# Kernel tuning notes

Hardware: AMD Instinct MI355X
Metric: run time of the kernel (lower is better)

## Reference

```python
import jax, jax.numpy as jnp
import numpy as np

E, N, D, H, F, M, L = 4, 2048, 256, 8, 2048, 4096, 3
GAMMA = 0.1
EPS = 1e-5  # torch LayerNorm default


def setup_inputs() -> dict:
    key = jax.random.key(0)
    ks = jax.random.split(key, 8)
    s = 0.02  # keep randn-initialized weights in a sane range
    return {
        "tokens": jax.random.normal(ks[0], (E, N, D), jnp.float32),
        "memories": jax.random.normal(ks[1], (L, M, D), jnp.float32),
        "in_proj_w": jax.random.normal(ks[2], (E, 3 * D, D), jnp.float32) * s,
        "in_proj_b": jnp.zeros((E, 3 * D), jnp.float32),
        "out_w": jax.random.normal(ks[3], (E, D, D), jnp.float32) * s,
        "out_b": jnp.zeros((E, D), jnp.float32),
        "lin1_w": jax.random.normal(ks[4], (E, F, D), jnp.float32) * s,
        "lin1_b": jnp.zeros((E, F), jnp.float32),
        "lin2_w": jax.random.normal(ks[5], (E, D, F), jnp.float32) * s,
        "lin2_b": jnp.zeros((E, D), jnp.float32),
        "ln1_w": jnp.ones((E, D), jnp.float32),
        "ln1_b": jnp.zeros((E, D), jnp.float32),
        "ln2_w": jnp.ones((E, D), jnp.float32),
        "ln2_b": jnp.zeros((E, D), jnp.float32),
        "agg_w": jax.random.normal(ks[6], (D, L * D), jnp.float32) * s,
        "agg_b": jnp.zeros((D,), jnp.float32),
        "global_gate": jax.random.normal(ks[7], (D, 1), jnp.float32),
    }


def _ln(x, g, b):
    mu = x.mean(-1, keepdims=True)
    var = ((x - mu) ** 2).mean(-1, keepdims=True)
    return (x - mu) * jax.lax.rsqrt(var + EPS) * g + b


def _mha(x, wqkv, bqkv, wo, bo):
    # unbatched nn.MultiheadAttention, self-attention, eval mode (no dropout)
    qkv = x @ wqkv.T + bqkv                          # [N, 3D]
    q, k, v = jnp.split(qkv, 3, axis=-1)
    hd = D // H
    q = q.reshape(-1, H, hd)
    k = k.reshape(-1, H, hd)
    v = v.reshape(-1, H, hd)
    att = jax.nn.softmax(jnp.einsum('nhd,mhd->hnm', q, k) / jnp.sqrt(jnp.float32(hd)), axis=-1)
    o = jnp.einsum('hnm,mhd->nhd', att, v).reshape(-1, D)
    return o @ wo.T + bo


def _forward(tokens, memories, in_proj_w, in_proj_b, out_w, out_b,
             lin1_w, lin1_b, lin2_w, lin2_b, ln1_w, ln1_b, ln2_w, ln2_b,
             agg_w, agg_b, global_gate):
    scale = 1.0 / jnp.sqrt(jnp.float32(D))
    # context for expert i = concat of all other experts' tokens  [E, (E-1)*N, D]
    contexts = jnp.stack([
        jnp.concatenate([tokens[j] for j in range(E) if j != i], axis=0)
        for i in range(E)
    ])

    def per_expert(tok, ctx, wqkv, bqkv, wo, bo, w1, b1, w2, b2, g1, be1, g2, be2):
        # cross-expert attention
        ca = jax.nn.softmax(tok @ ctx.T * scale, axis=-1) @ ctx
        x = tok + ca
        # one post-norm TransformerEncoderLayer (relu FFN, eval mode)
        x = _ln(x + _mha(x, wqkv, bqkv, wo, bo), g1, be1)
        x = _ln(x + (jax.nn.relu(x @ w1.T + b1) @ w2.T + b2), g2, be2)
        # multi-layer memory read + write accumulation
        scores = jax.nn.softmax(jnp.einsum('nd,lmd->lnm', x, memories) * scale, axis=-1)
        ret = jnp.einsum('lnm,lmd->lnd', scores, memories)        # [L, N, D]
        upd = jnp.einsum('lnm,nd->lmd', scores, x)                # [L, M, D]
        multi = ret.transpose(1, 0, 2).reshape(N, L * D) @ agg_w.T + agg_b
        return x + multi, upd

    expert_out, upds = jax.vmap(per_expert)(
        tokens, contexts, in_proj_w, in_proj_b, out_w, out_b,
        lin1_w, lin1_b, lin2_w, lin2_b, ln1_w, ln1_b, ln2_w, ln2_b)
    # EMA memory update (torch.no_grad -> stop_gradient)
    new_memories = jax.lax.stop_gradient((1.0 - GAMMA) * memories + GAMMA * upds.sum(0))
    # gated fusion
    pooled = expert_out.mean(axis=1)                              # [E, D]
    gate_weights = jax.nn.softmax((pooled @ global_gate).squeeze(-1), axis=0)
    fused = jnp.einsum('e,end->nd', gate_weights, expert_out)     # [N, D]
    return fused, gate_weights, new_memories


def reference(tokens, memories, in_proj_w, in_proj_b, out_w, out_b,
              lin1_w, lin1_b, lin2_w, lin2_b, ln1_w, ln1_b, ln2_w, ln2_b,
              agg_w, agg_b, global_gate):
    return _forward(tokens, memories, in_proj_w, in_proj_b, out_w, out_b,
                    lin1_w, lin1_b, lin2_w, lin2_b, ln1_w, ln1_b, ln2_w, ln2_b,
                    agg_w, agg_b, global_gate)
```

## Files before the change

kernel.cpp:

```cpp
#include <hip/hip_runtime.h>
#include <hip/hip_bf16.h>
#include <math.h>

#define E_ 4
#define N_ 2048
#define D_ 256
#define H_ 8
#define F_ 2048
#define M_ 4096
#define L_ 3
#define GAMMA_ 0.1f
#define EPS_ 1e-5f
#define CCH 8

#define GF_ATOMIC 1
#define GF_RELU   2

typedef __attribute__((ext_vector_type(8))) short  sh8;
typedef __attribute__((ext_vector_type(4))) float  fx4;
typedef __hip_bfloat16 bf16;

#define MFMA16 __builtin_amdgcn_mfma_f32_16x16x32_bf16

__device__ inline void gload_lds16(const void* g, void* l) {
    __builtin_amdgcn_global_load_lds((const __attribute__((address_space(1))) void*)g,
                                     (__attribute__((address_space(3))) void*)l, 16, 0, 0);
}

__device__ inline void stage_k64(const bf16* __restrict__ gbase, bf16* lds, int tid) {
    #pragma unroll
    for (int i = 0; i < 8; ++i) {
        int q = i * 256 + tid;
        int row = q >> 5, cst = q & 31;
        int cl = cst ^ (row & 7);
        gload_lds16((const char*)gbase + row * 512 + cl * 16, (char*)lds + q * 16);
    }
}
__device__ inline sh8 ldsK(const bf16* lds, int row, int ks, int hi) {
    return *(const sh8*)((const char*)lds + row * 512 + (((ks * 4 + hi) ^ (row & 7)) << 4));
}

__device__ inline void stage_v64(const bf16* __restrict__ gbase, long rstride, bf16* lds, int tid) {
    #pragma unroll
    for (int i = 0; i < 8; ++i) {
        int q = i * 256 + tid;
        int row = q >> 3, cst = q & 7;
        int cl = cst ^ (row & 7);
        gload_lds16((const char*)(gbase + (long)row * rstride + cl * 8), (char*)lds + q * 16);
    }
}
__device__ inline sh8 ldsV(const bf16* lds, int row, int ks, int hi) {
    return *(const sh8*)((const char*)lds + row * 128 + (((ks * 4 + hi) ^ (row & 7)) << 4));
}

template<int BN>
__global__ __launch_bounds__(256, 4)
void gemm_bf16(const bf16* __restrict__ A, int lda,
               const bf16* __restrict__ Bt, int ldb, long wstride,
               float* C, int ldc, bf16* Cbf,
               int M, int N, int K, int Kc,
               float alpha, const float* __restrict__ bias, long bstride,
               const float* res, int ldres, int flags,
               const bf16* __restrict__ zerobuf)
{
    constexpr int MI  = (BN == 128) ? 4 : 2;
    constexpr int BCH = BN * 8 / 256;
    __shared__ char smem[16384 + BN * 128];
    char* sA = smem;
    char* sB = smem + 16384;
    const int tid  = threadIdx.x;
    const int lane = tid & 63;
    const int lo   = lane & 15, hi = lane >> 4;
    const int wid  = tid >> 6;
    const int rowbase = (BN == 128) ? (wid >> 1) * 64 : wid * 32;
    const int colbase = (BN == 128) ? (wid & 1) * 64 : 0;
    const int bm = blockIdx.y * 128, bn = blockIdx.x * BN;

    const int eid = (blockIdx.y * 128) >> 11;
    const bf16* Bte = Bt + (long)eid * wstride;
    const float* biase = bias ? (bias + (long)eid * bstride) : nullptr;

    const int kbeg = blockIdx.z * Kc;
    const int kend = min(K, kbeg + Kc);

    fx4 acc[MI][4] = {};

    for (int k0 = kbeg; k0 < kend; k0 += 64) {
        #pragma unroll
        for (int i = 0; i < 4; ++i) {
            int id  = i * 256 + tid;
            int row = id >> 3;
            int c   = (id & 7) ^ (row & 7);
            int gk  = k0 + c * 8;
            const bf16* gp = (gk < kend) ? (A + (long)(bm + row) * lda + gk) : zerobuf;
            gload_lds16(gp, sA + id * 16);
        }
        #pragma unroll
        for (int i = 0; i < BCH; ++i) {
            int id  = i * 256 + tid;
            int row = id >> 3;
            int c   = (id & 7) ^ (row & 7);
            int gk  = k0 + c * 8;
            const bf16* gp = (gk < kend && bn + row < N) ? (Bte + (long)(bn + row) * ldb + gk)
                                                         : zerobuf;
            gload_lds16(gp, sB + id * 16);
        }
        asm volatile("s_waitcnt vmcnt(0)" ::: "memory");
        __syncthreads();

        #pragma unroll
        for (int kk = 0; kk < 2; ++kk) {
            const int ko = kk * 32 + hi * 8;
            sh8 af[MI], bfr[4];
            #pragma unroll
            for (int i = 0; i < MI; ++i) {
                int row = rowbase + i * 16 + lo;
                int off = (row * 128 + ko * 2) ^ ((row & 7) << 4);
                af[i] = *(const sh8*)(sA + off);
            }
            #pragma unroll
            for (int j = 0; j < 4; ++j) {
                int row = colbase + j * 16 + lo;
                int off = (row * 128 + ko * 2) ^ ((row & 7) << 4);
                bfr[j] = *(const sh8*)(sB + off);
            }
            #pragma unroll
            for (int i = 0; i < MI; ++i)
                #pragma unroll
                for (int j = 0; j < 4; ++j)
                    acc[i][j] = MFMA16(af[i], bfr[j], acc[i][j], 0, 0, 0);
        }
        __syncthreads();
    }

    const bool z0 = (blockIdx.z == 0);
// ... 32 lines not shown
    const int tid = threadIdx.x, lane = tid & 63, w = tid >> 6;
    const int lo = lane & 15, hi = lane >> 4;
    const float scaleH = 0.17677669529663687f;
    const bf16* qkv_e = qkv + (long)e * N_ * 768;
    const bf16* vT_eh = vT + ((long)e * D_ + h * 32) * N_;
    __shared__ bf16 Plds[4][16][72];

    sh8 qf = *(const sh8*)(qkv_e + (long)(n0 + w * 16 + lo) * 768 + h * 32 + hi * 8);

    float m[4], l[4];
    fx4 acc[2] = {};
    #pragma unroll
    for (int r = 0; r < 4; ++r) { m[r] = -INFINITY; l[r] = 0.f; }

    for (int kc = 0; kc < N_; kc += 64) {
        float sv[4][4], rmax[4], rsum[4];
        #pragma unroll
        for (int j = 0; j < 4; ++j) {
            sh8 kf = *(const sh8*)(qkv_e + (long)(kc + j * 16 + lo) * 768 + 256 + h * 32 + hi * 8);
            fx4 s = {};
            s = MFMA16(qf, kf, s, 0, 0, 0);
            #pragma unroll
            for (int r = 0; r < 4; ++r) sv[j][r] = s[r] * scaleH;
        }
        #pragma unroll
        for (int r = 0; r < 4; ++r)
            rmax[r] = fmaxf(fmaxf(sv[0][r], sv[1][r]), fmaxf(sv[2][r], sv[3][r]));
        #pragma unroll
        for (int d = 1; d < 16; d <<= 1)
            #pragma unroll
            for (int r = 0; r < 4; ++r) rmax[r] = fmaxf(rmax[r], __shfl_xor(rmax[r], d, 64));
        float sc[4];
        #pragma unroll
        for (int r = 0; r < 4; ++r) {
            float mn = fmaxf(m[r], rmax[r]);
            sc[r] = __expf(m[r] - mn);
            m[r] = mn; rsum[r] = 0.f;
        }
        #pragma unroll
        for (int j = 0; j < 4; ++j)
            #pragma unroll
            for (int r = 0; r < 4; ++r) {
                float p = __expf(sv[j][r] - m[r]);
                sv[j][r] = p; rsum[r] += p;
            }
        #pragma unroll
        for (int d = 1; d < 16; d <<= 1)
            #pragma unroll
            for (int r = 0; r < 4; ++r) rsum[r] += __shfl_xor(rsum[r], d, 64);
        #pragma unroll
        for (int r = 0; r < 4; ++r) l[r] = l[r] * sc[r] + rsum[r];
        #pragma unroll
        for (int j2 = 0; j2 < 2; ++j2)
            #pragma unroll
            for (int r = 0; r < 4; ++r) acc[j2][r] *= sc[r];
        #pragma unroll
        for (int j = 0; j < 4; ++j)
            #pragma unroll
            for (int r = 0; r < 4; ++r)
                Plds[w][hi * 4 + r][j * 16 + lo] = __float2bfloat16(sv[j][r]);
        asm volatile("s_waitcnt lgkmcnt(0)" ::: "memory");
        __builtin_amdgcn_sched_barrier(0);
        __builtin_amdgcn_s_setprio(1);
        #pragma unroll
        for (int ks = 0; ks < 2; ++ks) {
            sh8 pa = *(const sh8*)(&Plds[w][lo][ks * 32 + hi * 8]);
            #pragma unroll
            for (int j2 = 0; j2 < 2; ++j2) {
                sh8 vb = *(const sh8*)(vT_eh + (long)(j2 * 16 + lo) * N_ + kc + ks * 32 + hi * 8);
                acc[j2] = MFMA16(pa, vb, acc[j2], 0, 0, 0);
            }
        }
        __builtin_amdgcn_s_setprio(0);
    }
    #pragma unroll
    for (int j2 = 0; j2 < 2; ++j2)
        #pragma unroll
        for (int r = 0; r < 4; ++r) {
            long row = (long)e * N_ + n0 + w * 16 + hi * 4 + r;
            obuf[row * D_ + h * 32 + j2 * 16 + lo] = __float2bfloat16(acc[j2][r] / l[r]);
        }
}

__global__ __launch_bounds__(256, 2)
void flash_cross(const bf16* __restrict__ tok, const bf16* __restrict__ tokT,
                 bf16* __restrict__ Opart, float2* __restrict__ ml)
{
    const int e = blockIdx.z, ch = blockIdx.y;
    const int n0 = blockIdx.x * 64;
    const int tid = threadIdx.x, lane = tid & 63, w = tid >> 6;
    const int lo = lane & 15, hi = lane >> 4;
    const float scaleD = 1.0f / 16.0f;
    __shared__ bf16 Kt[64 * 256];
    __shared__ bf16 Vt[256 * 64];
    __shared__ bf16 Plds[4][16][72];

    sh8 qf[8];
    {
        const bf16* qr = tok + ((long)e * N_ + n0 + w * 16 + lo) * D_;
        #pragma unroll
        for (int ks = 0; ks < 8; ++ks) qf[ks] = *(const sh8*)(qr + ks * 32 + hi * 8);
    }
    float m[4], l[4];
    fx4 acc[16] = {};
    #pragma unroll
    for (int r = 0; r < 4; ++r) { m[r] = -INFINITY; l[r] = 0.f; }

    for (int kc = ch * 768; kc < ch * 768 + 768; kc += 64) {
        const int seg = kc >> 11;
        const int src = (seg < e) ? seg : seg + 1;
        const int rowb = kc & 2047;
        stage_k64(tok + ((long)src * N_ + rowb) * D_, Kt, tid);
        stage_v64(tokT + (long)src * D_ * N_ + rowb, N_, Vt, tid);
        asm volatile("s_waitcnt vmcnt(0)" ::: "memory");
        __syncthreads();

        float sv[4][4], rmax[4], rsum[4];
        __builtin_amdgcn_s_setprio(1);
        #pragma unroll
        for (int j = 0; j < 4; ++j) {
            int krow = j * 16 + lo;
            fx4 s = {};
            #pragma unroll
            for (int ks = 0; ks < 8; ++ks) {
                sh8 kf = ldsK(Kt, krow, ks, hi);
                s = MFMA16(qf[ks], kf, s, 0, 0, 0);
            }
            #pragma unroll
            for (int r = 0; r < 4; ++r) sv[j][r] = s[r] * scaleD;
        }
        __builtin_amdgcn_s_setprio(0);
        #pragma unroll
        for (int r = 0; r < 4; ++r)
            rmax[r] = fmaxf(fmaxf(sv[0][r], sv[1][r]), fmaxf(sv[2][r], sv[3][r]));
        #pragma unroll
        for (int d = 1; d < 16; d <<= 1)
            #pragma unroll
            for (int r = 0; r < 4; ++r) rmax[r] = fmaxf(rmax[r], __shfl_xor(rmax[r], d, 64));
        float sc[4];
        #pragma unroll
        for (int r = 0; r < 4; ++r) {
            float mn = fmaxf(m[r], rmax[r]);
            sc[r] = __expf(m[r] - mn);
            m[r] = mn; rsum[r] = 0.f;
        }
        #pragma unroll
        for (int j = 0; j < 4; ++j)
            #pragma unroll
            for (int r = 0; r < 4; ++r) {
                float p = __expf(sv[j][r] - m[r]);
                sv[j][r] = p; rsum[r] += p;
            }
        #pragma unroll
        for (int d = 1; d < 16; d <<= 1)
            #pragma unroll
            for (int r = 0; r < 4; ++r) rsum[r] += __shfl_xor(rsum[r], d, 64);
        #pragma unroll
        for (int r = 0; r < 4; ++r) l[r] = l[r] * sc[r] + rsum[r];
        #pragma unroll
        for (int j2 = 0; j2 < 16; ++j2)
            #pragma unroll
            for (int r = 0; r < 4; ++r) acc[j2][r] *= sc[r];
        #pragma unroll
        for (int j = 0; j < 4; ++j)
            #pragma unroll
            for (int r = 0; r < 4; ++r)
                Plds[w][hi * 4 + r][j * 16 + lo] = __float2bfloat16(sv[j][r]);
        asm volatile("s_waitcnt lgkmcnt(0)" ::: "memory");
        __builtin_amdgcn_sched_barrier(0);
        __builtin_amdgcn_s_setprio(1);
        #pragma unroll
        for (int ks = 0; ks < 2; ++ks) {
            sh8 pa = *(const sh8*)(&Plds[w][lo][ks * 32 + hi * 8]);
            #pragma unroll
            for (int j2 = 0; j2 < 16; ++j2) {
                sh8 vb = ldsV(Vt, j2 * 16 + lo, ks, hi);
                acc[j2] = MFMA16(pa, vb, acc[j2], 0, 0, 0);
            }
        }
        __builtin_amdgcn_s_setprio(0);
        __syncthreads();
    }
    const long base = (long)ch * E_ * N_ + (long)e * N_ + n0 + w * 16;
    #pragma unroll
    for (int j2 = 0; j2 < 16; ++j2)
        #pragma unroll
        for (int r = 0; r < 4; ++r)
            Opart[(base + hi * 4 + r) * D_ + j2 * 16 + lo] = __float2bfloat16(acc[j2][r] / l[r]);
    if (lo == 0) {
        #pragma unroll
        for (int r = 0; r < 4; ++r) {
            float2 t; t.x = m[r]; t.y = l[r];
            ml[base + hi * 4 + r] = t;
        }
    }
}

__global__ void cross_merge(const bf16* __restrict__ Opart, const float2* __restrict__ ml,
                            const float* __restrict__ tokens,
                            float* __restrict__ x0f, bf16* __restrict__ x0bf)
{
    long row = blockIdx.x; int d = threadIdx.x;
    float2 v[CCH];
    float mx = -INFINITY;
    #pragma unroll
    for (int i = 0; i < CCH; ++i) { v[i] = ml[(long)i * E_ * N_ + row]; mx = fmaxf(mx, v[i].x); }
    float L = 0.f, o = 0.f;
    #pragma unroll
    for (int i = 0; i < CCH; ++i) {
        float wgt = v[i].y * __expf(v[i].x - mx);
        L += wgt;
        o += wgt * __bfloat162float(Opart[((long)i * E_ * N_ + row) * D_ + d]);
    }
    float val = tokens[row * D_ + d] + o / L;
    x0f[row * D_ + d] = val;
    x0bf[row * D_ + d] = __float2bfloat16(val);
}

__global__ __launch_bounds__(256, 2)
void ret_flash(const bf16* __restrict__ x2b, const bf16* __restrict__ memb,
               const bf16* __restrict__ maggT, bf16* __restrict__ OmemH,
               float* __restrict__ rsH)
{
    const int li = blockIdx.y;
    const int e = blockIdx.z >> 1, mh = blockIdx.z & 1;
    const int n0 = blockIdx.x * 64;
    const int tid = threadIdx.x, lane = tid & 63, w = tid >> 6;
    const int lo = lane & 15, hi = lane >> 4;
    const float scaleD = 1.0f / 16.0f;
    __shared__ bf16 Kt[64 * 256];
    __shared__ bf16 Vt[256 * 64];
    __shared__ bf16 Plds[4][16][72];

    sh8 qf[8];
    {
        const bf16* qr = x2b + ((long)e * N_ + n0 + w * 16 + lo) * D_;
        #pragma unroll
        for (int ks = 0; ks < 8; ++ks) qf[ks] = *(const sh8*)(qr + ks * 32 + hi * 8);
    }
    float l[4] = {0.f, 0.f, 0.f, 0.f};
    fx4 acc[16] = {};
    const bf16* Kl = memb + (long)li * M_ * D_;
    const bf16* Vl = maggT + (long)li * D_ * M_;
    const int mbase = mh * 2048;

    for (int t = 0; t < 32; ++t) {
        const int m0 = mbase + t * 64;
        stage_k64(Kl + (long)m0 * D_, Kt, tid);
        stage_v64(Vl + m0, M_, Vt, tid);
        asm volatile("s_waitcnt vmcnt(0)" ::: "memory");
        __syncthreads();

        float sv[4][4], rsum[4] = {0.f, 0.f, 0.f, 0.f};
        __builtin_amdgcn_s_setprio(1);
        #pragma unroll
        for (int j = 0; j < 4; ++j) {
            int krow = j * 16 + lo;
            fx4 s = {};
            #pragma unroll
            for (int ks = 0; ks < 8; ++ks) {
                sh8 kf = ldsK(Kt, krow, ks, hi);
                s = MFMA16(qf[ks], kf, s, 0, 0, 0);
            }
            #pragma unroll
            for (int r = 0; r < 4; ++r) {
                float p = __expf(s[r] * scaleD);
                sv[j][r] = p; rsum[r] += p;
            }
        }
        __builtin_amdgcn_s_setprio(0);
        #pragma unroll
        for (int d = 1; d < 16; d <<= 1)
            #pragma unroll
            for (int r = 0; r < 4; ++r) rsum[r] += __shfl_xor(rsum[r], d, 64);
        #pragma unroll
        for (int r = 0; r < 4; ++r) l[r] += rsum[r];
        #pragma unroll
        for (int j = 0; j < 4; ++j)
            #pragma unroll
            for (int r = 0; r < 4; ++r)
                Plds[w][hi * 4 + r][j * 16 + lo] = __float2bfloat16(sv[j][r]);
        asm volatile("s_waitcnt lgkmcnt(0)" ::: "memory");
        __builtin_amdgcn_sched_barrier(0);
        __builtin_amdgcn_s_setprio(1);
        #pragma unroll
        for (int ks = 0; ks < 2; ++ks) {
            sh8 pa = *(const sh8*)(&Plds[w][lo][ks * 32 + hi * 8]);
            #pragma unroll
            for (int j2 = 0; j2 < 16; ++j2) {
                sh8 vb = ldsV(Vt, j2 * 16 + lo, ks, hi);
                acc[j2] = MFMA16(pa, vb, acc[j2], 0, 0, 0);
            }
        }
        __builtin_amdgcn_s_setprio(0);
        __syncthreads();
    }
    const long rowb = ((long)(mh * 12 + e * L_ + li)) * N_ + n0 + w * 16;
    #pragma unroll
    for (int j2 = 0; j2 < 16; ++j2)
        #pragma unroll
        for (int r = 0; r < 4; ++r)
            OmemH[(rowb + hi * 4 + r) * D_ + j2 * 16 + lo] = __float2bfloat16(acc[j2][r]);
    if (lo == 0) {
        #pragma unroll
        for (int r = 0; r < 4; ++r)
            rsH[rowb + hi * 4 + r] = l[r];
    }
}

__global__ __launch_bounds__(256, 2)
void upd_flash(const bf16* __restrict__ x2b, const bf16* __restrict__ memb,
               const bf16* __restrict__ x2T, const float* __restrict__ rsH,
               bf16* __restrict__ updpart)
{
    const int li = blockIdx.y, e = blockIdx.z;
    const int m0 = blockIdx.x * 64;
    const int tid = threadIdx.x, lane = tid & 63, w = tid >> 6;
    const int lo = lane & 15, hi = lane >> 4;
    const float scaleD = 1.0f / 16.0f;
    __shared__ bf16 Kt[64 * 256];
    __shared__ bf16 Vt[256 * 64];
    __shared__ bf16 Plds[4][16][72];

    sh8 qf[8];
    {
        const bf16* qr = memb + (long)li * M_ * D_ + (long)(m0 + w * 16 + lo) * D_;
        #pragma unroll
        for (int ks = 0; ks < 8; ++ks) qf[ks] = *(const sh8*)(qr + ks * 32 + hi * 8);
    }
    fx4 acc[16] = {};
    const float* rs0 = rsH + (long)(e * L_ + li) * N_;
    const float* rs1 = rsH + (long)(12 + e * L_ + li) * N_;
    const bf16* x2Te = x2T + (long)e * D_ * N_;

    for (int t = 0; t < 32; ++t) {
        const int n0 = t * 64;
        stage_k64(x2b + ((long)e * N_ + n0) * D_, Kt, tid);
        stage_v64(x2Te + n0, N_, Vt, tid);
        float rinv[4];
        #pragma unroll
        for (int j = 0; j < 4; ++j) {
            int n = n0 + j * 16 + lo;
            rinv[j] = 1.0f / (rs0[n] + rs1[n]);
        }
        asm volatile("s_waitcnt vmcnt(0)" ::: "memory");
        __syncthreads();

        __builtin_amdgcn_s_setprio(1);
        #pragma unroll
        for (int j = 0; j < 4; ++j) {
            int krow = j * 16 + lo;
            fx4 s = {};
            #pragma unroll
            for (int ks = 0; ks < 8; ++ks) {
                sh8 kf = ldsK(Kt, krow, ks, hi);
                s = MFMA16(qf[ks], kf, s, 0, 0, 0);
            }
            #pragma unroll
            for (int r = 0; r < 4; ++r) {
                float p = __expf(s[r] * scaleD) * rinv[j];
                Plds[w][hi * 4 + r][j * 16 + lo] = __float2bfloat16(p);
            }
        }
        __builtin_amdgcn_s_setprio(0);
        asm volatile("s_waitcnt lgkmcnt(0)" ::: "memory");
        __builtin_amdgcn_sched_barrier(0);
        __builtin_amdgcn_s_setprio(1);
        #pragma unroll
        for (int ks = 0; ks < 2; ++ks) {
            sh8 pa = *(const sh8*)(&Plds[w][lo][ks * 32 + hi * 8]);
            #pragma unroll
            for (int j2 = 0; j2 < 16; ++j2) {
                sh8 vb = ldsV(Vt, j2 * 16 + lo, ks, hi);
                acc[j2] = MFMA16(pa, vb, acc[j2], 0, 0, 0);
            }
        }
        __builtin_amdgcn_s_setprio(0);
        __syncthreads();
    }
    const long mrow = ((long)(e * L_ + li)) * M_ + m0 + w * 16;
    #pragma unroll
    for (int j2 = 0; j2 < 16; ++j2)
        #pragma unroll
        for (int r = 0; r < 4; ++r)
            updpart[(mrow + hi * 4 + r) * D_ + j2 * 16 + lo] = __float2bfloat16(acc[j2][r]);
}

__global__ void retscale(const bf16* __restrict__ OmemH, const float* __restrict__ rsH,
                         const float* __restrict__ aggb, float* __restrict__ xfinal)
{
    long row = blockIdx.x; int d = threadIdx.x;
    int e = (int)(row >> 11); long n = row & 2047;
    float s = aggb[d];
    #pragma unroll
    for (int li = 0; li < L_; ++li) {
        long r0 = ((long)(e * L_ + li)) * N_ + n;
        long r1 = ((long)(12 + e * L_ + li)) * N_ + n;
        float o = __bfloat162float(OmemH[r0 * D_ + d]) + __bfloat162float(OmemH[r1 * D_ + d]);
        s += o / (rsH[r0] + rsH[r1]);
    }
    xfinal[row * D_ + d] += s;
}

__global__ void layernorm_rows(const float* __restrict__ X, const float* __restrict__ g,
                               const float* __restrict__ b, float* __restrict__ out,
                               bf16* __restrict__ outbf)
{
    __shared__ float red[256];
    int row = blockIdx.x, t = threadIdx.x;
    int e = row >> 11;
    float v = X[(long)row * 256 + t];
    red[t] = v; __syncthreads();
    for (int s = 128; s > 0; s >>= 1) { if (t < s) red[t] += red[t + s]; __syncthreads(); }
    float mu = red[0] * (1.0f / 256.0f); __syncthreads();
    float d = v - mu;
    red[t] = d * d; __syncthreads();
    for (int s = 128; s > 0; s >>= 1) { if (t < s) red[t] += red[t + s]; __syncthreads(); }
    float var = red[0] * (1.0f / 256.0f);
    float o = d * rsqrtf(var + EPS_) * g[e * 256 + t] + b[e * 256 + t];
    out[(long)row * 256 + t] = o;
    outbf[(long)row * 256 + t] = __float2bfloat16(o);
}

__global__ void cvt_bf16(const float* __restrict__ in, bf16* __restrict__ out, long n) {
    long i = ((long)blockIdx.x * 256 + threadIdx.x) * 4;
    if (i < n) {
        float4 v = *(const float4*)(in + i);
        out[i + 0] = __float2bfloat16(v.x);
        out[i + 1] = __float2bfloat16(v.y);
        out[i + 2] = __float2bfloat16(v.z);
        out[i + 3] = __float2bfloat16(v.w);
    }
}

__device__ inline float ldf(const float* p) { return *p; }
__device__ inline float ldf(const bf16* p)  { return __bfloat162float(*p); }

template<typename T>
__global__ void transpose_bf16(const T* __restrict__ in, bf16* __restrict__ out,
                               int R, int C, int ldin, int ldout) {
    __shared__ float t[64][65];
    int tx = threadIdx.x & 63, ty = threadIdx.x >> 6;
    int r0 = blockIdx.y * 64, c0 = blockIdx.x * 64;
    #pragma unroll
    for (int i = 0; i < 16; ++i) {
        int r = ty + i * 4;
        t[r][tx] = ldf(&in[(long)(r0 + r) * ldin + (c0 + tx)]);
    }
    __syncthreads();
    #pragma unroll
    for (int i = 0; i < 16; ++i) {
        int c = ty + i * 4;
        out[(long)(c0 + c) * ldout + (r0 + tx)] = __float2bfloat16(t[tx][c]);
    }
}

__global__ void mem_update(const float4* __restrict__ mem, const bf16* __restrict__ updpart,
                           float4* __restrict__ out) {
    long i = (long)blockIdx.x * 256 + threadIdx.x;
    const long LMD = (long)L_ * M_ * D_;
    if (i < LMD / 4) {
// ... 81 lines not shown
    cvt_bf16<<<dim3((unsigned)((n / 4 + 255) / 256)), dim3(256), 0, s>>>(in, out, n);
}

extern "C" void kernel_launch(void* const* d_in, const int* in_sizes, int n_in,
                              void* d_out, int out_size, void* d_ws, size_t ws_size,
                              hipStream_t stream) {
    const float* tokens    = (const float*)d_in[0];
    const float* memories  = (const float*)d_in[1];
    const float* in_proj_w = (const float*)d_in[2];
    const float* in_proj_b = (const float*)d_in[3];
    const float* out_w     = (const float*)d_in[4];
    const float* out_b     = (const float*)d_in[5];
    const float* lin1_w    = (const float*)d_in[6];
    const float* lin1_b    = (const float*)d_in[7];
    const float* lin2_w    = (const float*)d_in[8];
    const float* lin2_b    = (const float*)d_in[9];
    const float* ln1_w     = (const float*)d_in[10];
    const float* ln1_b     = (const float*)d_in[11];
    const float* ln2_w     = (const float*)d_in[12];
    const float* ln2_b     = (const float*)d_in[13];
    const float* agg_w     = (const float*)d_in[14];
    const float* agg_b     = (const float*)d_in[15];
    const float* gg        = (const float*)d_in[16];

    char* p = (char*)d_ws;
    auto alloc = [&](size_t bytes) { char* r = p; p += (bytes + 255) & ~(size_t)255; return r; };

    char*  regionA = alloc((size_t)32 * 1024 * 1024);
    bf16*  Opart   = (bf16*)regionA;
    bf16*  hid_all = (bf16*)regionA;
    bf16*  OmemH   = (bf16*)regionA;

    char*  regionB = alloc((size_t)32 * 1024 * 1024);
    bf16*  qkv_bf  = (bf16*)regionB;
    bf16*  vT_bf   = (bf16*)(regionB + 12582912);
    bf16*  obuf_bf = (bf16*)(regionB + 12582912 + 4194304);
    bf16*  updpart = (bf16*)regionB;

    float* xfinal  = (float*)alloc((size_t)E_ * N_ * D_ * 4);
    bf16*  x2_bf   = (bf16*)alloc((size_t)E_ * N_ * D_ * 2);
    bf16*  x2T_bf  = (bf16*)alloc((size_t)E_ * D_ * N_ * 2);
    float* x0f     = (float*)alloc((size_t)E_ * N_ * D_ * 4);
    bf16*  x0bf    = (bf16*)alloc((size_t)E_ * N_ * D_ * 2);
    float* ybuf    = (float*)alloc((size_t)E_ * N_ * D_ * 4);
    bf16*  tok_bf  = (bf16*)alloc((size_t)E_ * N_ * D_ * 2);
    bf16*  tokT_bf = (bf16*)alloc((size_t)E_ * D_ * N_ * 2);
    bf16*  mem_bf  = (bf16*)alloc((size_t)L_ * M_ * D_ * 2);
    bf16*  maggT   = (bf16*)alloc((size_t)L_ * D_ * M_ * 2);
    float2* mlbuf  = (float2*)alloc((size_t)CCH * E_ * N_ * sizeof(float2));
    float* rsH     = (float*)alloc((size_t)2 * 12 * N_ * 4);
    bf16*  ipw_bf  = (bf16*)alloc((size_t)E_ * 3 * D_ * D_ * 2);
    bf16*  outw_bf = (bf16*)alloc((size_t)E_ * D_ * D_ * 2);
    bf16*  l1w_bf  = (bf16*)alloc((size_t)E_ * F_ * D_ * 2);
    bf16*  l2w_bf  = (bf16*)alloc((size_t)E_ * D_ * F_ * 2);
    bf16*  aggw_bf = (bf16*)alloc((size_t)D_ * 3 * D_ * 2);
    float* pooled  = (float*)alloc(1024 * 4);
    float* gatebuf = (float*)alloc(64);
    bf16*  zerobuf = (bf16*)alloc(64);

    float* x1f  = x0f;
    bf16*  x1bf = x0bf;

    float* out_fused = (float*)d_out;
    float* out_gate  = out_fused + (long)N_ * D_;
    float* out_mem   = out_gate + E_;

    hipMemsetAsync(zerobuf, 0, 64, stream);
    hipMemsetAsync(pooled, 0, 1024 * 4, stream);

    convert(stream, tokens, tok_bf, (long)E_ * N_ * D_);
    convert(stream, memories, mem_bf, (long)L_ * M_ * D_);
    convert(stream, in_proj_w, ipw_bf, (long)E_ * 3 * D_ * D_);
    convert(stream, out_w, outw_bf, (long)E_ * D_ * D_);
    convert(stream, lin1_w, l1w_bf, (long)E_ * F_ * D_);
    convert(stream, lin2_w, l2w_bf, (long)E_ * D_ * F_);
    convert(stream, agg_w, aggw_bf, (long)D_ * 3 * D_);
    for (int e = 0; e < E_; ++e)
        transposeF(stream, tokens + (long)e * N_ * D_, tokT_bf + (long)e * D_ * N_, N_, D_, D_, N_);
    for (int l = 0; l < L_; ++l)
        gemm(stream, 128, aggw_bf + l * D_, 3 * D_, mem_bf + (long)l * M_ * D_, D_, 0,
             nullptr, M_, maggT + (long)l * D_ * M_, D_, M_, D_, D_,
             1.0f, nullptr, 0, nullptr, 0, 0, zerobuf);

    flash_cross<<<dim3(N_ / 64, CCH, E_), dim3(256), 0, stream>>>(tok_bf, tokT_bf, Opart, mlbuf);
    cross_merge<<<dim3(E_ * N_), dim3(256), 0, stream>>>(Opart, mlbuf, tokens, x0f, x0bf);

    gemm(stream, 128, x0bf, D_, ipw_bf, D_, (long)3 * D_ * D_,
         nullptr, 3 * D_, qkv_bf, E_ * N_, 3 * D_, D_, D_,
         1.0f, in_proj_b, 3 * D_, nullptr, 0, 0, zerobuf);
    for (int e = 0; e < E_; ++e)
        transposeB(stream, qkv_bf + (long)e * N_ * 3 * D_ + 2 * D_, vT_bf + (long)e * D_ * N_,
                   N_, D_, 3 * D_, N_);
    flash_mha<<<dim3(N_ / 64, H_, E_), dim3(256), 0, stream>>>(qkv_bf, vT_bf, obuf_bf);
    gemm(stream, 64, obuf_bf, D_, outw_bf, D_, (long)D_ * D_,
         ybuf, D_, nullptr, E_ * N_, D_, D_, D_,
         1.0f, out_b, D_, x0f, D_, 0, zerobuf);
    layernorm_rows<<<dim3(E_ * N_), dim3(256), 0, stream>>>(ybuf, ln1_w, ln1_b, x1f, x1bf);

    gemm(stream, 128, x1bf, D_, l1w_bf, D_, (long)F_ * D_,
         nullptr, F_, hid_all, E_ * N_, F_, D_, D_,
         1.0f, lin1_b, F_, nullptr, 0, GF_RELU, zerobuf);
    hipMemsetAsync(ybuf, 0, (size_t)E_ * N_ * D_ * 4, stream);
    gemm(stream, 64, hid_all, F_, l2w_bf, F_, (long)D_ * F_,
         ybuf, D_, nullptr, E_ * N_, D_, F_, 512,
         1.0f, lin2_b, D_, x1f, D_, GF_ATOMIC, zerobuf);
    layernorm_rows<<<dim3(E_ * N_), dim3(256), 0, stream>>>(ybuf, ln2_w, ln2_b, xfinal, x2_bf);
    for (int e = 0; e < E_; ++e)
        transposeF(stream, xfinal + (long)e * N_ * D_, x2T_bf + (long)e * D_ * N_, N_, D_, D_, N_);

    ret_flash<<<dim3(N_ / 64, L_, E_ * 2), dim3(256), 0, stream>>>(x2_bf, mem_bf, maggT, OmemH, rsH);
    upd_flash<<<dim3(M_ / 64, L_, E_), dim3(256), 0, stream>>>(x2_bf, mem_bf, x2T_bf, rsH, updpart);
    retscale<<<dim3(E_ * N_), dim3(256), 0, stream>>>(OmemH, rsH, agg_b, xfinal);

    mem_update<<<dim3(L_ * M_ * D_ / 4 / 256), dim3(256), 0, stream>>>(
        (const float4*)memories, updpart, (float4*)out_mem);
    pool_partial<<<dim3(E_, 16), dim3(256), 0, stream>>>(xfinal, pooled);
    gate_kernel<<<dim3(1), dim3(256), 0, stream>>>(pooled, gg, out_gate, gatebuf);
    fuse_kernel<<<dim3((N_ * D_ + 255) / 256), dim3(256), 0, stream>>>(xfinal, gatebuf, out_fused);
}
```

Measured before the change: 876.0 us.

## Double-buffer K/V tiles in flash kernels with 32-row chunks

The three flash-attention style kernels (cross attention, memory retrieval, memory update) now stage K and V in 32-row chunks into two LDS buffers. The next chunk's global-to-LDS loads are issued right after the barrier so they overlap with compute on the current chunk, and the trailing barrier is removed. This targets the load latency that was exposed because each iteration waited on its own loads before computing. The cost is twice as many loop iterations with smaller MFMA batches per iteration and more barrier and softmax bookkeeping overhead. LDS use stays the same size.

```diff
diff --git a/kernel.cpp b/kernel.cpp
--- a/kernel.cpp
+++ b/kernel.cpp
@@ -36,21 +36,30 @@
         gload_lds16((const char*)gbase + row * 512 + cl * 16, (char*)lds + q * 16);
     }
 }
+__device__ inline void stage_k32(const bf16* __restrict__ gbase, bf16* lds, int tid) {
+    #pragma unroll
+    for (int i = 0; i < 4; ++i) {
+        int q = i * 256 + tid;
+        int row = q >> 5, cst = q & 31;
+        int cl = cst ^ (row & 7);
+        gload_lds16((const char*)gbase + row * 512 + cl * 16, (char*)lds + q * 16);
+    }
+}
 __device__ inline sh8 ldsK(const bf16* lds, int row, int ks, int hi) {
     return *(const sh8*)((const char*)lds + row * 512 + (((ks * 4 + hi) ^ (row & 7)) << 4));
 }
 
-__device__ inline void stage_v64(const bf16* __restrict__ gbase, long rstride, bf16* lds, int tid) {
-    #pragma unroll
-    for (int i = 0; i < 8; ++i) {
+__device__ inline void stage_v32(const bf16* __restrict__ gbase, long rstride, bf16* lds, int tid) {
+    #pragma unroll
+    for (int i = 0; i < 4; ++i) {
         int q = i * 256 + tid;
-        int row = q >> 3, cst = q & 7;
-        int cl = cst ^ (row & 7);
+        int row = q >> 2, cst = q & 3;
+        int cl = cst ^ (row & 3);
         gload_lds16((const char*)(gbase + (long)row * rstride + cl * 8), (char*)lds + q * 16);
     }
 }
-__device__ inline sh8 ldsV(const bf16* lds, int row, int ks, int hi) {
-    return *(const sh8*)((const char*)lds + row * 128 + (((ks * 4 + hi) ^ (row & 7)) << 4));
+__device__ inline sh8 ldsV32(const bf16* lds, int row, int hi) {
+    return *(const sh8*)((const char*)lds + row * 64 + ((hi ^ (row & 3)) << 4));
 }
 
 template<int BN>
@@ -258,9 +267,9 @@
     const int tid = threadIdx.x, lane = tid & 63, w = tid >> 6;
     const int lo = lane & 15, hi = lane >> 4;
     const float scaleD = 1.0f / 16.0f;
-    __shared__ bf16 Kt[64 * 256];
-    __shared__ bf16 Vt[256 * 64];
-    __shared__ bf16 Plds[4][16][72];
+    __shared__ bf16 Kt[2][32 * 256];
+    __shared__ bf16 Vt[2][256 * 32];
+    __shared__ bf16 Plds[4][16][40];
 
     sh8 qf[8];
     {
@@ -273,24 +282,36 @@
     #pragma unroll
     for (int r = 0; r < 4; ++r) { m[r] = -INFINITY; l[r] = 0.f; }
 
-    for (int kc = ch * 768; kc < ch * 768 + 768; kc += 64) {
-        const int seg = kc >> 11;
-        const int src = (seg < e) ? seg : seg + 1;
-        const int rowb = kc & 2047;
-        stage_k64(tok + ((long)src * N_ + rowb) * D_, Kt, tid);
-        stage_v64(tokT + (long)src * D_ * N_ + rowb, N_, Vt, tid);
+    const int kc0 = ch * 768;
+    {
+        int seg = kc0 >> 11; int src = (seg < e) ? seg : seg + 1;
+        int rowb = kc0 & 2047;
+        stage_k32(tok + ((long)src * N_ + rowb) * D_, Kt[0], tid);
+        stage_v32(tokT + (long)src * D_ * N_ + rowb, N_, Vt[0], tid);
+    }
+    for (int t = 0; t < 24; ++t) {
+        const int b = t & 1;
         asm volatile("s_waitcnt vmcnt(0)" ::: "memory");
         __syncthreads();
-
-        float sv[4][4], rmax[4], rsum[4];
+        if (t + 1 < 24) {
+            int kc2 = kc0 + (t + 1) * 32;
+            int seg2 = kc2 >> 11; int src2 = (seg2 < e) ? seg2 : seg2 + 1;
+            int rowb2 = kc2 & 2047;
+            stage_k32(tok + ((long)src2 * N_ + rowb2) * D_, Kt[b ^ 1], tid);
+            stage_v32(tokT + (long)src2 * D_ * N_ + rowb2, N_, Vt[b ^ 1], tid);
+        }
+        const bf16* Ktc = Kt[b];
+        const bf16* Vtc = Vt[b];
+
+        float sv[2][4], rmax[4], rsum[4];
         __builtin_amdgcn_s_setprio(1);
         #pragma unroll
-        for (int j = 0; j < 4; ++j) {
+        for (int j = 0; j < 2; ++j) {
             int krow = j * 16 + lo;
             fx4 s = {};
             #pragma unroll
             for (int ks = 0; ks < 8; ++ks) {
-                sh8 kf = ldsK(Kt, krow, ks, hi);
+                sh8 kf = ldsK(Ktc, krow, ks, hi);
                 s = MFMA16(qf[ks], kf, s, 0, 0, 0);
             }
             #pragma unroll
@@ -298,8 +319,7 @@
         }
         __builtin_amdgcn_s_setprio(0);
         #pragma unroll
-        for (int r = 0; r < 4; ++r)
-            rmax[r] = fmaxf(fmaxf(sv[0][r], sv[1][r]), fmaxf(sv[2][r], sv[3][r]));
+        for (int r = 0; r < 4; ++r) rmax[r] = fmaxf(sv[0][r], sv[1][r]);
         #pragma unroll
         for (int d = 1; d < 16; d <<= 1)
             #pragma unroll
@@ -312,7 +332,7 @@
             m[r] = mn; rsum[r] = 0.f;
         }
         #pragma unroll
-        for (int j = 0; j < 4; ++j)
+        for (int j = 0; j < 2; ++j)
             #pragma unroll
             for (int r = 0; r < 4; ++r) {
                 float p = __expf(sv[j][r] - m[r]);
@@ -329,24 +349,22 @@
             #pragma unroll
             for (int r = 0; r < 4; ++r) acc[j2][r] *= sc[r];
         #pragma unroll
-        for (int j = 0; j < 4; ++j)
+        for (int j = 0; j < 2; ++j)
             #pragma unroll
             for (int r = 0; r < 4; ++r)
                 Plds[w][hi * 4 + r][j * 16 + lo] = __float2bfloat16(sv[j][r]);
         asm volatile("s_waitcnt lgkmcnt(0)" ::: "memory");
         __builtin_amdgcn_sched_barrier(0);
         __builtin_amdgcn_s_setprio(1);
-        #pragma unroll
-        for (int ks = 0; ks < 2; ++ks) {
-            sh8 pa = *(const sh8*)(&Plds[w][lo][ks * 32 + hi * 8]);
+        {
+            sh8 pa = *(const sh8*)(&Plds[w][lo][hi * 8]);
             #pragma unroll
             for (int j2 = 0; j2 < 16; ++j2) {
-                sh8 vb = ldsV(Vt, j2 * 16 + lo, ks, hi);
+                sh8 vb = ldsV32(Vtc, j2 * 16 + lo, hi);
                 acc[j2] = MFMA16(pa, vb, acc[j2], 0, 0, 0);
             }
         }
         __builtin_amdgcn_s_setprio(0);
-        __syncthreads();
     }
     const long base = (long)ch * E_ * N_ + (long)e * N_ + n0 + w * 16;
     #pragma unroll
@@ -395,9 +413,9 @@
     const int tid = threadIdx.x, lane = tid & 63, w = tid >> 6;
     const int lo = lane & 15, hi = lane >> 4;
     const float scaleD = 1.0f / 16.0f;
-    __shared__ bf16 Kt[64 * 256];
-    __shared__ bf16 Vt[256 * 64];
-    __shared__ bf16 Plds[4][16][72];
+    __shared__ bf16 Kt[2][32 * 256];
+    __shared__ bf16 Vt[2][256 * 32];
+    __shared__ bf16 Plds[4][16][40];
 
     sh8 qf[8];
     {
@@ -411,22 +429,29 @@
     const bf16* Vl = maggT + (long)li * D_ * M_;
     const int mbase = mh * 2048;
 
-    for (int t = 0; t < 32; ++t) {
-        const int m0 = mbase + t * 64;
-        stage_k64(Kl + (long)m0 * D_, Kt, tid);
-        stage_v64(Vl + m0, M_, Vt, tid);
+    stage_k32(Kl + (long)mbase * D_, Kt[0], tid);
+    stage_v32(Vl + mbase, M_, Vt[0], tid);
+    for (int t = 0; t < 64; ++t) {
+        const int b = t & 1;
         asm volatile("s_waitcnt vmcnt(0)" ::: "memory");
         __syncthreads();
-
-        float sv[4][4], rsum[4] = {0.f, 0.f, 0.f, 0.f};
+        if (t + 1 < 64) {
+            const int m1 = mbase + (t + 1) * 32;
+            stage_k32(Kl + (long)m1 * D_, Kt[b ^ 1], tid);
+            stage_v32(Vl + m1, M_, Vt[b ^ 1], tid);
+        }
+        const bf16* Ktc = Kt[b];
+        const bf16* Vtc = Vt[b];
+
+        float sv[2][4], rsum[4] = {0.f, 0.f, 0.f, 0.f};
         __builtin_amdgcn_s_setprio(1);
         #pragma unroll
-        for (int j = 0; j < 4; ++j) {
+        for (int j = 0; j < 2; ++j) {
             int krow = j * 16 + lo;
             fx4 s = {};
             #pragma unroll
             for (int ks = 0; ks < 8; ++ks) {
-                sh8 kf = ldsK(Kt, krow, ks, hi);
+                sh8 kf = ldsK(Ktc, krow, ks, hi);
                 s = MFMA16(qf[ks], kf, s, 0, 0, 0);
             }
             #pragma unroll
@@ -443,24 +468,22 @@
         #pragma unroll
         for (int r = 0; r < 4; ++r) l[r] += rsum[r];
         #pragma unroll
-        for (int j = 0; j < 4; ++j)
+        for (int j = 0; j < 2; ++j)
             #pragma unroll
             for (int r = 0; r < 4; ++r)
                 Plds[w][hi * 4 + r][j * 16 + lo] = __float2bfloat16(sv[j][r]);
         asm volatile("s_waitcnt lgkmcnt(0)" ::: "memory");
         __builtin_amdgcn_sched_barrier(0);
         __builtin_amdgcn_s_setprio(1);
-        #pragma unroll
-        for (int ks = 0; ks < 2; ++ks) {
-            sh8 pa = *(const sh8*)(&Plds[w][lo][ks * 32 + hi * 8]);
+        {
+            sh8 pa = *(const sh8*)(&Plds[w][lo][hi * 8]);
             #pragma unroll
             for (int j2 = 0; j2 < 16; ++j2) {
-                sh8 vb = ldsV(Vt, j2 * 16 + lo, ks, hi);
+                sh8 vb = ldsV32(Vtc, j2 * 16 + lo, hi);
                 acc[j2] = MFMA16(pa, vb, acc[j2], 0, 0, 0);
             }
         }
         __builtin_amdgcn_s_setprio(0);
-        __syncthreads();
     }
     const long rowb = ((long)(mh * 12 + e * L_ + li)) * N_ + n0 + w * 16;
     #pragma unroll
@@ -485,9 +508,9 @@
     const int tid = threadIdx.x, lane = tid & 63, w = tid >> 6;
     const int lo = lane & 15, hi = lane >> 4;
     const float scaleD = 1.0f / 16.0f;
-    __shared__ bf16 Kt[64 * 256];
-    __shared__ bf16 Vt[256 * 64];
-    __shared__ bf16 Plds[4][16][72];
+    __shared__ bf16 Kt[2][32 * 256];
+    __shared__ bf16 Vt[2][256 * 32];
+    __shared__ bf16 Plds[4][16][40];
 
     sh8 qf[8];
     {
@@ -500,27 +523,35 @@
     const float* rs1 = rsH + (long)(12 + e * L_ + li) * N_;
     const bf16* x2Te = x2T + (long)e * D_ * N_;
 
-    for (int t = 0; t < 32; ++t) {
-        const int n0 = t * 64;
-        stage_k64(x2b + ((long)e * N_ + n0) * D_, Kt, tid);
-        stage_v64(x2Te + n0, N_, Vt, tid);
-        float rinv[4];
-        #pragma unroll
-        for (int j = 0; j < 4; ++j) {
+    stage_k32(x2b + (long)e * N_ * D_, Kt[0], tid);
+    stage_v32(x2Te, N_, Vt[0], tid);
+    for (int t = 0; t < 64; ++t) {
+        const int b = t & 1;
+        const int n0 = t * 32;
+        float rinv[2];
+        #pragma unroll
+        for (int j = 0; j < 2; ++j) {
             int n = n0 + j * 16 + lo;
             rinv[j] = 1.0f / (rs0[n] + rs1[n]);
         }
         asm volatile("s_waitcnt vmcnt(0)" ::: "memory");
         __syncthreads();
+        if (t + 1 < 64) {
+            const int n1 = (t + 1) * 32;
+            stage_k32(x2b + ((long)e * N_ + n1) * D_, Kt[b ^ 1], tid);
+            stage_v32(x2Te + n1, N_, Vt[b ^ 1], tid);
+        }
+        const bf16* Ktc = Kt[b];
+        const bf16* Vtc = Vt[b];
 
         __builtin_amdgcn_s_setprio(1);
         #pragma unroll
-        for (int j = 0; j < 4; ++j) {
+        for (int j = 0; j < 2; ++j) {
             int krow = j * 16 + lo;
             fx4 s = {};
             #pragma unroll
             for (int ks = 0; ks < 8; ++ks) {
-                sh8 kf = ldsK(Kt, krow, ks, hi);
+                sh8 kf = ldsK(Ktc, krow, ks, hi);
                 s = MFMA16(qf[ks], kf, s, 0, 0, 0);
             }
             #pragma unroll
@@ -533,17 +564,15 @@
         asm volatile("s_waitcnt lgkmcnt(0)" ::: "memory");
         __builtin_amdgcn_sched_barrier(0);
         __builtin_amdgcn_s_setprio(1);
-        #pragma unroll
-        for (int ks = 0; ks < 2; ++ks) {
-            sh8 pa = *(const sh8*)(&Plds[w][lo][ks * 32 + hi * 8]);
+        {
+            sh8 pa = *(const sh8*)(&Plds[w][lo][hi * 8]);
             #pragma unroll
             for (int j2 = 0; j2 < 16; ++j2) {
-                sh8 vb = ldsV(Vt, j2 * 16 + lo, ks, hi);
+                sh8 vb = ldsV32(Vtc, j2 * 16 + lo, hi);
                 acc[j2] = MFMA16(pa, vb, acc[j2], 0, 0, 0);
             }
         }
         __builtin_amdgcn_s_setprio(0);
-        __syncthreads();
     }
     const long mrow = ((long)(e * L_ + li)) * M_ + m0 + w * 16;
     #pragma unroll
```

Measured after the change: 985.9 us. 12.5% more time.

## Double-buffer K/V tiles and widen flash kernels to 8 waves

Applied to the files above, without the earlier changes.

The three flash-style kernels (flash_cross, ret_flash, upd_flash) now run 512 threads per block, covering 128 query rows. The K/V tiles are double-buffered in LDS, and the next tile is prefetched right after the barrier, so the global-to-LDS copy overlaps the MFMA work and the trailing barrier is removed. Each staged K/V tile is now shared by twice as many query rows, which halves staging traffic per row. The cost is that LDS use grows to roughly 146KB per block, so only one block fits per CU, and the grids have half as many blocks.

```diff
diff --git a/kernel.cpp b/kernel.cpp
--- a/kernel.cpp
+++ b/kernel.cpp
@@ -36,18 +36,26 @@
         gload_lds16((const char*)gbase + row * 512 + cl * 16, (char*)lds + q * 16);
     }
 }
-__device__ inline sh8 ldsK(const bf16* lds, int row, int ks, int hi) {
-    return *(const sh8*)((const char*)lds + row * 512 + (((ks * 4 + hi) ^ (row & 7)) << 4));
-}
-
-__device__ inline void stage_v64(const bf16* __restrict__ gbase, long rstride, bf16* lds, int tid) {
-    #pragma unroll
-    for (int i = 0; i < 8; ++i) {
-        int q = i * 256 + tid;
+__device__ inline void stage_k64w8(const bf16* __restrict__ gbase, bf16* lds, int tid) {
+    #pragma unroll
+    for (int i = 0; i < 4; ++i) {
+        int q = i * 512 + tid;
+        int row = q >> 5, cst = q & 31;
+        int cl = cst ^ (row & 7);
+        gload_lds16((const char*)gbase + row * 512 + cl * 16, (char*)lds + q * 16);
+    }
+}
+__device__ inline void stage_v64w8(const bf16* __restrict__ gbase, long rstride, bf16* lds, int tid) {
+    #pragma unroll
+    for (int i = 0; i < 4; ++i) {
+        int q = i * 512 + tid;
         int row = q >> 3, cst = q & 7;
         int cl = cst ^ (row & 7);
         gload_lds16((const char*)(gbase + (long)row * rstride + cl * 8), (char*)lds + q * 16);
     }
+}
+__device__ inline sh8 ldsK(const bf16* lds, int row, int ks, int hi) {
+    return *(const sh8*)((const char*)lds + row * 512 + (((ks * 4 + hi) ^ (row & 7)) << 4));
 }
 __device__ inline sh8 ldsV(const bf16* lds, int row, int ks, int hi) {
     return *(const sh8*)((const char*)lds + row * 128 + (((ks * 4 + hi) ^ (row & 7)) << 4));
@@ -249,18 +257,18 @@
         }
 }
 
-__global__ __launch_bounds__(256, 2)
+__global__ __launch_bounds__(512, 2)
 void flash_cross(const bf16* __restrict__ tok, const bf16* __restrict__ tokT,
                  bf16* __restrict__ Opart, float2* __restrict__ ml)
 {
     const int e = blockIdx.z, ch = blockIdx.y;
-    const int n0 = blockIdx.x * 64;
+    const int n0 = blockIdx.x * 128;
     const int tid = threadIdx.x, lane = tid & 63, w = tid >> 6;
     const int lo = lane & 15, hi = lane >> 4;
     const float scaleD = 1.0f / 16.0f;
-    __shared__ bf16 Kt[64 * 256];
-    __shared__ bf16 Vt[256 * 64];
-    __shared__ bf16 Plds[4][16][72];
+    __shared__ bf16 Kt[2][64 * 256];
+    __shared__ bf16 Vt[2][256 * 64];
+    __shared__ bf16 Plds[8][16][72];
 
     sh8 qf[8];
     {
@@ -273,14 +281,26 @@
     #pragma unroll
     for (int r = 0; r < 4; ++r) { m[r] = -INFINITY; l[r] = 0.f; }
 
-    for (int kc = ch * 768; kc < ch * 768 + 768; kc += 64) {
-        const int seg = kc >> 11;
-        const int src = (seg < e) ? seg : seg + 1;
-        const int rowb = kc & 2047;
-        stage_k64(tok + ((long)src * N_ + rowb) * D_, Kt, tid);
-        stage_v64(tokT + (long)src * D_ * N_ + rowb, N_, Vt, tid);
+    const int kc0 = ch * 768;
+    {
+        int seg = kc0 >> 11; int src = (seg < e) ? seg : seg + 1;
+        int rowb = kc0 & 2047;
+        stage_k64w8(tok + ((long)src * N_ + rowb) * D_, Kt[0], tid);
+        stage_v64w8(tokT + (long)src * D_ * N_ + rowb, N_, Vt[0], tid);
+    }
+    for (int t = 0; t < 12; ++t) {
+        const int b = t & 1;
         asm volatile("s_waitcnt vmcnt(0)" ::: "memory");
         __syncthreads();
+        if (t + 1 < 12) {
+            int kc2 = kc0 + (t + 1) * 64;
+            int seg2 = kc2 >> 11; int src2 = (seg2 < e) ? seg2 : seg2 + 1;
+            int rowb2 = kc2 & 2047;
+            stage_k64w8(tok + ((long)src2 * N_ + rowb2) * D_, Kt[b ^ 1], tid);
+            stage_v64w8(tokT + (long)src2 * D_ * N_ + rowb2, N_, Vt[b ^ 1], tid);
+        }
+        const bf16* Ktc = Kt[b];
+        const bf16* Vtc = Vt[b];
 
         float sv[4][4], rmax[4], rsum[4];
         __builtin_amdgcn_s_setprio(1);
@@ -290,7 +310,7 @@
             fx4 s = {};
             #pragma unroll
             for (int ks = 0; ks < 8; ++ks) {
-                sh8 kf = ldsK(Kt, krow, ks, hi);
+                sh8 kf = ldsK(Ktc, krow, ks, hi);
                 s = MFMA16(qf[ks], kf, s, 0, 0, 0);
             }
             #pragma unroll
@@ -341,12 +361,11 @@
             sh8 pa = *(const sh8*)(&Plds[w][lo][ks * 32 + hi * 8]);
             #pragma unroll
             for (int j2 = 0; j2 < 16; ++j2) {
-                sh8 vb = ldsV(Vt, j2 * 16 + lo, ks, hi);
+                sh8 vb = ldsV(Vtc, j2 * 16 + lo, ks, hi);
                 acc[j2] = MFMA16(pa, vb, acc[j2], 0, 0, 0);
             }
         }
         __builtin_amdgcn_s_setprio(0);
-        __syncthreads();
     }
     const long base = (long)ch * E_ * N_ + (long)e * N_ + n0 + w * 16;
     #pragma unroll
@@ -384,20 +403,20 @@
     x0bf[row * D_ + d] = __float2bfloat16(val);
 }
 
-__global__ __launch_bounds__(256, 2)
+__global__ __launch_bounds__(512, 2)
 void ret_flash(const bf16* __restrict__ x2b, const bf16* __restrict__ memb,
                const bf16* __restrict__ maggT, bf16* __restrict__ OmemH,
                float* __restrict__ rsH)
 {
     const int li = blockIdx.y;
     const int e = blockIdx.z >> 1, mh = blockIdx.z & 1;
-    const int n0 = blockIdx.x * 64;
+    const int n0 = blockIdx.x * 128;
     const int tid = threadIdx.x, lane = tid & 63, w = tid >> 6;
     const int lo = lane & 15, hi = lane >> 4;
     const float scaleD = 1.0f / 16.0f;
-    __shared__ bf16 Kt[64 * 256];
-    __shared__ bf16 Vt[256 * 64];
-    __shared__ bf16 Plds[4][16][72];
+    __shared__ bf16 Kt[2][64 * 256];
+    __shared__ bf16 Vt[2][256 * 64];
+    __shared__ bf16 Plds[8][16][72];
 
     sh8 qf[8];
     {
@@ -411,12 +430,19 @@
     const bf16* Vl = maggT + (long)li * D_ * M_;
     const int mbase = mh * 2048;
 
+    stage_k64w8(Kl + (long)mbase * D_, Kt[0], tid);
+    stage_v64w8(Vl + mbase, M_, Vt[0], tid);
     for (int t = 0; t < 32; ++t) {
-        const int m0 = mbase + t * 64;
-        stage_k64(Kl + (long)m0 * D_, Kt, tid);
-        stage_v64(Vl + m0, M_, Vt, tid);
+        const int b = t & 1;
         asm volatile("s_waitcnt vmcnt(0)" ::: "memory");
         __syncthreads();
+        if (t + 1 < 32) {
+            const int m1 = mbase + (t + 1) * 64;
+            stage_k64w8(Kl + (long)m1 * D_, Kt[b ^ 1], tid);
+            stage_v64w8(Vl + m1, M_, Vt[b ^ 1], tid);
+        }
+        const bf16* Ktc = Kt[b];
+        const bf16* Vtc = Vt[b];
 
         float sv[4][4], rsum[4] = {0.f, 0.f, 0.f, 0.f};
         __builtin_amdgcn_s_setprio(1);
@@ -426,7 +452,7 @@
             fx4 s = {};
             #pragma unroll
             for (int ks = 0; ks < 8; ++ks) {
-                sh8 kf = ldsK(Kt, krow, ks, hi);
+                sh8 kf = ldsK(Ktc, krow, ks, hi);
                 s = MFMA16(qf[ks], kf, s, 0, 0, 0);
             }
             #pragma unroll
@@ -455,12 +481,11 @@
             sh8 pa = *(const sh8*)(&Plds[w][lo][ks * 32 + hi * 8]);
             #pragma unroll
             for (int j2 = 0; j2 < 16; ++j2) {
-                sh8 vb = ldsV(Vt, j2 * 16 + lo, ks, hi);
+                sh8 vb = ldsV(Vtc, j2 * 16 + lo, ks, hi);
                 acc[j2] = MFMA16(pa, vb, acc[j2], 0, 0, 0);
             }
         }
         __builtin_amdgcn_s_setprio(0);
-        __syncthreads();
     }
     const long rowb = ((long)(mh * 12 + e * L_ + li)) * N_ + n0 + w * 16;
     #pragma unroll
@@ -475,19 +500,19 @@
     }
 }
 
-__global__ __launch_bounds__(256, 2)
+__global__ __launch_bounds__(512, 2)
 void upd_flash(const bf16* __restrict__ x2b, const bf16* __restrict__ memb,
                const bf16* __restrict__ x2T, const float* __restrict__ rsH,
                bf16* __restrict__ updpart)
 {
     const int li = blockIdx.y, e = blockIdx.z;
-    const int m0 = blockIdx.x * 64;
+    const int m0 = blockIdx.x * 128;
     const int tid = threadIdx.x, lane = tid & 63, w = tid >> 6;
     const int lo = lane & 15, hi = lane >> 4;
     const float scaleD = 1.0f / 16.0f;
-    __shared__ bf16 Kt[64 * 256];
-    __shared__ bf16 Vt[256 * 64];
-    __shared__ bf16 Plds[4][16][72];
+    __shared__ bf16 Kt[2][64 * 256];
+    __shared__ bf16 Vt[2][256 * 64];
+    __shared__ bf16 Plds[8][16][72];
 
     sh8 qf[8];
     {
@@ -500,10 +525,11 @@
     const float* rs1 = rsH + (long)(12 + e * L_ + li) * N_;
     const bf16* x2Te = x2T + (long)e * D_ * N_;
 
+    stage_k64w8(x2b + (long)e * N_ * D_, Kt[0], tid);
+    stage_v64w8(x2Te, N_, Vt[0], tid);
     for (int t = 0; t < 32; ++t) {
+        const int b = t & 1;
         const int n0 = t * 64;
-        stage_k64(x2b + ((long)e * N_ + n0) * D_, Kt, tid);
-        stage_v64(x2Te + n0, N_, Vt, tid);
         float rinv[4];
         #pragma unroll
         for (int j = 0; j < 4; ++j) {
@@ -512,6 +538,13 @@
         }
         asm volatile("s_waitcnt vmcnt(0)" ::: "memory");
         __syncthreads();
+        if (t + 1 < 32) {
+            const int n1 = (t + 1) * 64;
+            stage_k64w8(x2b + ((long)e * N_ + n1) * D_, Kt[b ^ 1], tid);
+            stage_v64w8(x2Te + n1, N_, Vt[b ^ 1], tid);
+        }
+        const bf16* Ktc = Kt[b];
+        const bf16* Vtc = Vt[b];
 
         __builtin_amdgcn_s_setprio(1);
         #pragma unroll
@@ -520,7 +553,7 @@
             fx4 s = {};
             #pragma unroll
             for (int ks = 0; ks < 8; ++ks) {
-                sh8 kf = ldsK(Kt, krow, ks, hi);
+                sh8 kf = ldsK(Ktc, krow, ks, hi);
                 s = MFMA16(qf[ks], kf, s, 0, 0, 0);
             }
             #pragma unroll
@@ -538,12 +571,11 @@
             sh8 pa = *(const sh8*)(&Plds[w][lo][ks * 32 + hi * 8]);
             #pragma unroll
             for (int j2 = 0; j2 < 16; ++j2) {
-                sh8 vb = ldsV(Vt, j2 * 16 + lo, ks, hi);
+                sh8 vb = ldsV(Vtc, j2 * 16 + lo, ks, hi);
                 acc[j2] = MFMA16(pa, vb, acc[j2], 0, 0, 0);
             }
         }
         __builtin_amdgcn_s_setprio(0);
-        __syncthreads();
     }
     const long mrow = ((long)(e * L_ + li)) * M_ + m0 + w * 16;
     #pragma unroll
@@ -791,7 +823,7 @@
              nullptr, M_, maggT + (long)l * D_ * M_, D_, M_, D_, D_,
              1.0f, nullptr, 0, nullptr, 0, 0, zerobuf);
 
-    flash_cross<<<dim3(N_ / 64, CCH, E_), dim3(256), 0, stream>>>(tok_bf, tokT_bf, Opart, mlbuf);
+    flash_cross<<<dim3(N_ / 128, CCH, E_), dim3(512), 0, stream>>>(tok_bf, tokT_bf, Opart, mlbuf);
     cross_merge<<<dim3(E_ * N_), dim3(256), 0, stream>>>(Opart, mlbuf, tokens, x0f, x0bf);
 
     gemm(stream, 128, x0bf, D_, ipw_bf, D_, (long)3 * D_ * D_,
@@ -817,8 +849,8 @@
     for (int e = 0; e < E_; ++e)
         transposeF(stream, xfinal + (long)e * N_ * D_, x2T_bf + (long)e * D_ * N_, N_, D_, D_, N_);
 
-    ret_flash<<<dim3(N_ / 64, L_, E_ * 2), dim3(256), 0, stream>>>(x2_bf, mem_bf, maggT, OmemH, rsH);
-    upd_flash<<<dim3(M_ / 64, L_, E_), dim3(256), 0, stream>>>(x2_bf, mem_bf, x2T_bf, rsH, updpart);
+    ret_flash<<<dim3(N_ / 128, L_, E_ * 2), dim3(512), 0, stream>>>(x2_bf, mem_bf, maggT, OmemH, rsH);
+    upd_flash<<<dim3(M_ / 128, L_, E_), dim3(512), 0, stream>>>(x2_bf, mem_bf, x2T_bf, rsH, updpart);
     retscale<<<dim3(E_ * N_), dim3(256), 0, stream>>>(OmemH, rsH, agg_b, xfinal);
 
     mem_update<<<dim3(L_ * M_ * D_ / 4 / 256), dim3(256), 0, stream>>>(
```

Result: no change. 888.7 us (+1.5%).
